# Optimization experiments

Measured on AMD Instinct MI355X. Metric: run time of the kernel, lower is better.

Reference implementation:

```python
import jax, jax.numpy as jnp
import numpy as np

E = 8        # num_workers / experts
D = 1024     # decoder_embed_dim
F = 4096     # decoder_ffn_embed_dim
S, B = 2048, 2
LN_EPS = 1e-5


def setup_inputs() -> dict:
    key = jax.random.key(0)
    ks = jax.random.split(key, 8)
    scale_in = 1.0 / np.sqrt(D)
    scale_ff = 1.0 / np.sqrt(F)
    return {
        "input_features": jax.random.normal(ks[0], (S, B, D), dtype=jnp.float32),
        "centroids": jax.random.normal(ks[1], (E, D), dtype=jnp.float32) * scale_in,  # Linear(D, E, bias=False) weight
        "ln_g": jnp.ones((E, D), dtype=jnp.float32),
        "ln_b": jnp.zeros((E, D), dtype=jnp.float32),
        "W1": jax.random.normal(ks[2], (E, D, F), dtype=jnp.float32) * scale_in,
        "b1": jax.random.normal(ks[3], (E, F), dtype=jnp.float32) * 0.01,
        "W2": jax.random.normal(ks[4], (E, F, D), dtype=jnp.float32) * scale_ff,  # original zero-inits; random for non-trivial reference
        "b2": jax.random.normal(ks[5], (E, D), dtype=jnp.float32) * 0.01,
    }


def _moe_forward(input_features, centroids, ln_g, ln_b, W1, b1, W2, b2):
    s, b, d = input_features.shape
    # [S,B,D] -> transpose(0,1) -> [B,S,D] -> flatten tokens
    x = jnp.swapaxes(input_features, 0, 1).reshape(-1, d)  # [T, D]
    # fp32 gating, top-1 (greedy) assignment; BASE layer does NOT scale by gate prob
    logits = x.astype(jnp.float32) @ centroids.astype(jnp.float32).T  # [T, E]
    assign = jnp.argmax(logits, axis=-1)                              # [T]
    onehot = jax.nn.one_hot(assign, E, dtype=x.dtype)                 # [T, E]
    # dispatch: zero out tokens not assigned to expert e  -> [E, T, D]
    disp = jnp.einsum("te,td->etd", onehot, x)
    # expert-local MoESublayer: xs + ff2(relu(ff1(LN(xs))))
    mu = disp.mean(-1, keepdims=True)
    var = disp.var(-1, keepdims=True)
    xn = (disp - mu) * jax.lax.rsqrt(var + LN_EPS)
    xn = xn * ln_g[:, None, :] + ln_b[:, None, :]
    h = jax.nn.relu(jnp.einsum("etd,edf->etf", xn, W1) + b1[:, None, :])
    y = jnp.einsum("etf,efd->etd", h, W2) + b2[:, None, :]
    y = disp + y  # residual
    # combine: pick assigned expert's output per token (sort+all2all+inverse-sort == identity permutation here)
    out = jnp.einsum("te,etd->td", onehot, y)  # [T, D]
    return jnp.swapaxes(out.reshape(b, s, d), 0, 1)  # back to [S, B, D]


def reference(input_features, centroids, ln_g, ln_b, W1, b1, W2, b2):
    return _moe_forward(input_features, centroids, ln_g, ln_b, W1, b1, W2, b2)
```

## Files before the change

kernel.cpp:

```cpp
#include <hip/hip_runtime.h>
#include <hip/hip_bf16.h>

#define E_ 8
#define D_ 1024
#define F_ 4096
#define S_ 2048
#define B_ 2
#define T_ 4096
#define LN_EPS 1e-5f
#define MAXTAB 40

typedef __attribute__((ext_vector_type(8))) short short8;
typedef __attribute__((ext_vector_type(4))) float f32x4;

__device__ __forceinline__ unsigned short f2bf(float f) {
  __hip_bfloat16 h = __float2bfloat16(f);
  return *reinterpret_cast<unsigned short*>(&h);
}

__device__ __forceinline__ void gload_lds16(const void* g, void* l) {
  __builtin_amdgcn_global_load_lds((const __attribute__((address_space(1))) void*)g,
                                   (__attribute__((address_space(3))) void*)l,
                                   16, 0, 0);
}

__global__ __launch_bounds__(256) void gate_kernel(const float* __restrict__ x,
    const float* __restrict__ cent, int* __restrict__ assign_, int* __restrict__ counts) {
  int token = blockIdx.x * 4 + (threadIdx.x >> 6);
  int lane = threadIdx.x & 63;
  int s = token & (S_ - 1);
  int b = token >> 11;
  const float* xr = x + ((size_t)s * B_ + b) * D_;
  float acc[E_];
#pragma unroll
  for (int e = 0; e < E_; ++e) acc[e] = 0.f;
#pragma unroll
  for (int c = 0; c < 4; ++c) {
    f32x4 xv = *(const f32x4*)(xr + c * 256 + lane * 4);
#pragma unroll
    for (int e = 0; e < E_; ++e) {
      f32x4 cv = *(const f32x4*)(cent + e * D_ + c * 256 + lane * 4);
      acc[e] += xv.x * cv.x + xv.y * cv.y + xv.z * cv.z + xv.w * cv.w;
    }
  }
#pragma unroll
  for (int off = 32; off > 0; off >>= 1) {
#pragma unroll
    for (int e = 0; e < E_; ++e) acc[e] += __shfl_down(acc[e], off);
  }
  if (lane == 0) {
    int best = 0; float bv = acc[0];
#pragma unroll
    for (int e = 1; e < E_; ++e) if (acc[e] > bv) { bv = acc[e]; best = e; }
    assign_[token] = best;
    atomicAdd(&counts[best], 1);
  }
}

__global__ void prefix_kernel(const int* __restrict__ counts, int* __restrict__ offs,
                              int* __restrict__ cursor, int* __restrict__ tab) {
  if (threadIdx.x == 0) {
    int s = 0, t = 0;
    for (int e = 0; e < E_; ++e) {
      offs[e] = s; cursor[e] = s;
      int nb = (counts[e] + 127) >> 7;
      for (int m = 0; m < nb; ++m) tab[t++] = (e << 16) | m;
      s += counts[e];
    }
    offs[E_] = s;
    for (; t < MAXTAB; ++t) tab[t] = -1;
  }
}

__global__ __launch_bounds__(256) void ln_scatter_kernel(const float* __restrict__ x,
    const float* __restrict__ g_, const float* __restrict__ bb_,
    const float* __restrict__ b2_,
    const int* __restrict__ assign_, int* __restrict__ cursor,
    int* __restrict__ perm, unsigned short* __restrict__ Xb,
    float* __restrict__ outp) {
  int token = blockIdx.x * 4 + (threadIdx.x >> 6);
  int lane = threadIdx.x & 63;
  int s = token & (S_ - 1), b = token >> 11;
  const float* xr = x + ((size_t)s * B_ + b) * D_;
  float* orow = outp + ((size_t)s * B_ + b) * D_;
  float v[16];
  float sum = 0.f, sq = 0.f;
#pragma unroll
  for (int c = 0; c < 4; ++c) {
    f32x4 xv = *(const f32x4*)(xr + c * 256 + lane * 4);
    v[c * 4 + 0] = xv.x; v[c * 4 + 1] = xv.y; v[c * 4 + 2] = xv.z; v[c * 4 + 3] = xv.w;
    sum += xv.x + xv.y + xv.z + xv.w;
    sq += xv.x * xv.x + xv.y * xv.y + xv.z * xv.z + xv.w * xv.w;
  }
#pragma unroll
  for (int off = 32; off > 0; off >>= 1) {
    sum += __shfl_down(sum, off);
    sq += __shfl_down(sq, off);
  }
  sum = __shfl(sum, 0); sq = __shfl(sq, 0);
  float mu = sum * (1.f / D_);
  float var = sq * (1.f / D_) - mu * mu;
  float rstd = rsqrtf(var + LN_EPS);
  int e = assign_[token];
  int slot = 0;
  if (lane == 0) { slot = atomicAdd(&cursor[e], 1); perm[slot] = token; }
  slot = __shfl(slot, 0);
  unsigned short* dst = Xb + (size_t)slot * D_;
#pragma unroll
  for (int c = 0; c < 4; ++c) {
    int d = c * 256 + lane * 4;
    f32x4 gv = *(const f32x4*)(g_ + e * D_ + d);
    f32x4 bv = *(const f32x4*)(bb_ + e * D_ + d);
    f32x4 b2v = *(const f32x4*)(b2_ + e * D_ + d);
    ushort4 o;
    o.x = f2bf((v[c * 4 + 0] - mu) * rstd * gv.x + bv.x);
    o.y = f2bf((v[c * 4 + 1] - mu) * rstd * gv.y + bv.y);
    o.z = f2bf((v[c * 4 + 2] - mu) * rstd * gv.z + bv.z);
    o.w = f2bf((v[c * 4 + 3] - mu) * rstd * gv.w + bv.w);
    *(ushort4*)(dst + d) = o;
    f32x4 oi;
    oi.x = v[c * 4 + 0] + b2v.x; oi.y = v[c * 4 + 1] + b2v.y;
    oi.z = v[c * 4 + 2] + b2v.z; oi.w = v[c * 4 + 3] + b2v.w;
    *(f32x4*)(orow + d) = oi;
  }
}

template <int K, int N, int MODE, int KSPLIT>
__global__ __launch_bounds__(256) void moe_gemm_kernel(
    const unsigned short* __restrict__ A,
    const float* __restrict__ W,
    const float* __restrict__ bias,
    const int* __restrict__ offs,
    const int* __restrict__ tab,
    const int* __restrict__ perm,
    void* __restrict__ outp) {
  const int tentry = tab[blockIdx.y];
  if (tentry < 0) return;
  const int e = tentry >> 16;
  const int m0 = (tentry & 0xffff) << 7;
  const int off = offs[e];
  const int cnt = offs[e + 1] - off;
  const int n0 = blockIdx.x * 128;
  const int kstart = blockIdx.z * (K / KSPLIT);
  constexpr int NSTEP = (K / KSPLIT) / 32;

  const int tid = threadIdx.x;
  const int lane = tid & 63;
  const int wave = tid >> 6;

  __shared__ __align__(16) unsigned short lA[4096];
  __shared__ __align__(16) unsigned short lB[4096];

  const int ar = tid & 127;
  const int aq0 = tid >> 7;
  const int arow = off + min(m0 + ar, cnt - 1);
  const unsigned short* ap = A + (size_t)arow * K + kstart;
  unsigned short* ldst0 = lA + (0 * 256 + wave * 64) * 8;
  unsigned short* ldst1 = lA + (1 * 256 + wave * 64) * 8;

  const int bq = wave;
  const int bn = (tid & 63) * 2;
  const float* wp = W + (size_t)e * K * N + (size_t)(kstart + bq * 8) * N + n0 + bn;
  unsigned short* bdst = lB + bq * 1024 + bn * 8;

  f32x4 acc[4][4] = {};
  const int wr = (wave >> 1) * 64;
  const int wc = (wave & 1) * 64;
  const int fr = lane & 15;
  const int fq = lane >> 4;
  const unsigned short* fA = lA + fq * 1024 + (wr + fr) * 8;
  const unsigned short* fB = lB + fq * 1024 + (wc + fr) * 8;

  float2 br[8];
#pragma unroll
  for (int j = 0; j < 8; ++j) br[j] = *(const float2*)(wp + (size_t)j * N);

  for (int s = 0; s < NSTEP; ++s) {
    __syncthreads();
    short8 c0, c1;
#pragma unroll
    for (int j = 0; j < 8; ++j) {
      c0[j] = (short)f2bf(br[j].x);
      c1[j] = (short)f2bf(br[j].y);
    }
    *(short8*)(bdst) = c0;
    *(short8*)(bdst + 8) = c1;
    gload_lds16(ap + s * 32 + aq0 * 8, ldst0);
    gload_lds16(ap + s * 32 + (aq0 + 2) * 8, ldst1);
    __syncthreads();
    short8 af[4], bf[4];
#pragma unroll
    for (int m = 0; m < 4; ++m) af[m] = *(const short8*)(fA + m * 128);
#pragma unroll
    for (int n = 0; n < 4; ++n) bf[n] = *(const short8*)(fB + n * 128);
    if (s + 1 < NSTEP) {
      const float* wp2 = wp + (size_t)(s + 1) * 32 * N;
#pragma unroll
      for (int j = 0; j < 8; ++j) br[j] = *(const float2*)(wp2 + (size_t)j * N);
    }
#pragma unroll
    for (int m = 0; m < 4; ++m) {
#pragma unroll
      for (int n = 0; n < 4; ++n)
        acc[m][n] = __builtin_amdgcn_mfma_f32_16x16x32_bf16(af[m], bf[n], acc[m][n], 0, 0, 0);
    }
  }

  if (MODE == 0) {
    unsigned short* Hout = (unsigned short*)outp;
    float bv[4];
#pragma unroll
    for (int n = 0; n < 4; ++n) bv[n] = bias[e * N + n0 + wc + n * 16 + fr];
#pragma unroll
    for (int m = 0; m < 4; ++m) {
#pragma unroll
      for (int j = 0; j < 4; ++j) {
        int rg = m0 + wr + m * 16 + fq * 4 + j;
        if (rg < cnt) {
          size_t base = (size_t)(off + rg) * N;
#pragma unroll
          for (int n = 0; n < 4; ++n) {
            float hv = acc[m][n][j] + bv[n];
            hv = fmaxf(hv, 0.f);
            Hout[base + n0 + wc + n * 16 + fr] = f2bf(hv);
          }
        }
      }
    }
  } else {
    float* Out = (float*)outp;
#pragma unroll
    for (int m = 0; m < 4; ++m) {
#pragma unroll
      for (int j = 0; j < 4; ++j) {
        int rg = m0 + wr + m * 16 + fq * 4 + j;
        if (rg < cnt) {
          int token = perm[off + rg];
          size_t base = ((size_t)(token & (S_ - 1)) * B_ + (token >> 11)) * (size_t)D_;
#pragma unroll
          for (int n = 0; n < 4; ++n)
            atomicAdd(&Out[base + n0 + wc + n * 16 + fr], acc[m][n][j]);
        }
      }
    }
  }
}

extern "C" void kernel_launch(void* const* d_in, const int* in_sizes, int n_in,
                              void* d_out, int out_size, void* d_ws, size_t ws_size,
                              hipStream_t stream) {
  const float* x    = (const float*)d_in[0];
  const float* cent = (const float*)d_in[1];
  const float* lng  = (const float*)d_in[2];
  const float* lnb  = (const float*)d_in[3];
  const float* W1   = (const float*)d_in[4];
  const float* b1   = (const float*)d_in[5];
  const float* W2   = (const float*)d_in[6];
  const float* b2   = (const float*)d_in[7];
  float* out = (float*)d_out;

  char* ws = (char*)d_ws;
  int* counts  = (int*)(ws + 0);
  int* offs    = (int*)(ws + 64);
  int* cursor  = (int*)(ws + 128);
  int* tab     = (int*)(ws + 256);
  int* perm    = (int*)(ws + 4096);
  int* assign_ = (int*)(ws + 4096 + 4 * T_);
  unsigned short* Xb = (unsigned short*)(ws + ((size_t)1 << 16));
  unsigned short* H  = (unsigned short*)(ws + ((size_t)1 << 24));

  if (ws_size < ((size_t)1 << 26)) return;

  hipMemsetAsync(counts, 0, 64, stream);
  gate_kernel<<<T_ / 4, 256, 0, stream>>>(x, cent, assign_, counts);
  prefix_kernel<<<1, 64, 0, stream>>>(counts, offs, cursor, tab);
  ln_scatter_kernel<<<T_ / 4, 256, 0, stream>>>(x, lng, lnb, b2, assign_, cursor, perm, Xb, out);
  moe_gemm_kernel<D_, F_, 0, 1><<<dim3(F_ / 128, MAXTAB, 1), 256, 0, stream>>>(
      Xb, W1, b1, offs, tab, perm, (void*)H);
  moe_gemm_kernel<F_, D_, 1, 2><<<dim3(D_ / 128, MAXTAB, 2), 256, 0, stream>>>(
      H, W2, nullptr, offs, tab, perm, (void*)out);
}
```

Before: 348.2 us.

## Fuse gating into LN scatter with fixed-capacity buckets and double-buffer GEMM LDS

Merges the gate and LN/scatter kernels into one pass that computes logits, picks an expert, claims a slot in a per-expert fixed-capacity bucket (CAP=1024) and writes the normalized bf16 row, which removes one read of x and the assign round trip. The GEMM kernel now double-buffers A and B tiles in LDS and prefetches the next k-step while running MFMAs, so it needs one barrier per step instead of two. The B load pattern changes to scalar strided loads per lane. The fixed capacity assumes no expert gets more than 1024 tokens; a heavier expert would overflow its bucket and be wrong.

```diff
diff --git a/kernel.cpp b/kernel.cpp
--- a/kernel.cpp
+++ b/kernel.cpp
@@ -7,6 +7,7 @@
 #define S_ 2048
 #define B_ 2
 #define T_ 4096
+#define CAP 1024
 #define LN_EPS 1e-5f
 #define MAXTAB 40
 
@@ -24,66 +25,22 @@
                                    16, 0, 0);
 }
 
-__global__ __launch_bounds__(256) void gate_kernel(const float* __restrict__ x,
-    const float* __restrict__ cent, int* __restrict__ assign_, int* __restrict__ counts) {
-  int token = blockIdx.x * 4 + (threadIdx.x >> 6);
-  int lane = threadIdx.x & 63;
-  int s = token & (S_ - 1);
-  int b = token >> 11;
-  const float* xr = x + ((size_t)s * B_ + b) * D_;
-  float acc[E_];
-#pragma unroll
-  for (int e = 0; e < E_; ++e) acc[e] = 0.f;
-#pragma unroll
-  for (int c = 0; c < 4; ++c) {
-    f32x4 xv = *(const f32x4*)(xr + c * 256 + lane * 4);
-#pragma unroll
-    for (int e = 0; e < E_; ++e) {
-      f32x4 cv = *(const f32x4*)(cent + e * D_ + c * 256 + lane * 4);
-      acc[e] += xv.x * cv.x + xv.y * cv.y + xv.z * cv.z + xv.w * cv.w;
-    }
-  }
-#pragma unroll
-  for (int off = 32; off > 0; off >>= 1) {
-#pragma unroll
-    for (int e = 0; e < E_; ++e) acc[e] += __shfl_down(acc[e], off);
-  }
-  if (lane == 0) {
-    int best = 0; float bv = acc[0];
-#pragma unroll
-    for (int e = 1; e < E_; ++e) if (acc[e] > bv) { bv = acc[e]; best = e; }
-    assign_[token] = best;
-    atomicAdd(&counts[best], 1);
-  }
-}
-
-__global__ void prefix_kernel(const int* __restrict__ counts, int* __restrict__ offs,
-                              int* __restrict__ cursor, int* __restrict__ tab) {
-  if (threadIdx.x == 0) {
-    int s = 0, t = 0;
-    for (int e = 0; e < E_; ++e) {
-      offs[e] = s; cursor[e] = s;
-      int nb = (counts[e] + 127) >> 7;
-      for (int m = 0; m < nb; ++m) tab[t++] = (e << 16) | m;
-      s += counts[e];
-    }
-    offs[E_] = s;
-    for (; t < MAXTAB; ++t) tab[t] = -1;
-  }
-}
-
-__global__ __launch_bounds__(256) void ln_scatter_kernel(const float* __restrict__ x,
+__global__ __launch_bounds__(256) void gate_ln_kernel(
+    const float* __restrict__ x, const float* __restrict__ cent,
     const float* __restrict__ g_, const float* __restrict__ bb_,
     const float* __restrict__ b2_,
-    const int* __restrict__ assign_, int* __restrict__ cursor,
-    int* __restrict__ perm, unsigned short* __restrict__ Xb,
-    float* __restrict__ outp) {
+    int* __restrict__ counts, int* __restrict__ perm,
+    unsigned short* __restrict__ Xb, float* __restrict__ outp) {
   int token = blockIdx.x * 4 + (threadIdx.x >> 6);
   int lane = threadIdx.x & 63;
   int s = token & (S_ - 1), b = token >> 11;
   const float* xr = x + ((size_t)s * B_ + b) * D_;
   float* orow = outp + ((size_t)s * B_ + b) * D_;
+
   float v[16];
+  float acc[E_];
+#pragma unroll
+  for (int e = 0; e < E_; ++e) acc[e] = 0.f;
   float sum = 0.f, sq = 0.f;
 #pragma unroll
   for (int c = 0; c < 4; ++c) {
@@ -91,21 +48,34 @@
     v[c * 4 + 0] = xv.x; v[c * 4 + 1] = xv.y; v[c * 4 + 2] = xv.z; v[c * 4 + 3] = xv.w;
     sum += xv.x + xv.y + xv.z + xv.w;
     sq += xv.x * xv.x + xv.y * xv.y + xv.z * xv.z + xv.w * xv.w;
+#pragma unroll
+    for (int e = 0; e < E_; ++e) {
+      f32x4 cv = *(const f32x4*)(cent + e * D_ + c * 256 + lane * 4);
+      acc[e] += xv.x * cv.x + xv.y * cv.y + xv.z * cv.z + xv.w * cv.w;
+    }
   }
 #pragma unroll
   for (int off = 32; off > 0; off >>= 1) {
     sum += __shfl_down(sum, off);
     sq += __shfl_down(sq, off);
-  }
+#pragma unroll
+    for (int e = 0; e < E_; ++e) acc[e] += __shfl_down(acc[e], off);
+  }
+  int best = 0, slot = 0;
+  if (lane == 0) {
+    float bv = acc[0];
+#pragma unroll
+    for (int e = 1; e < E_; ++e) if (acc[e] > bv) { bv = acc[e]; best = e; }
+    slot = atomicAdd(&counts[best], 1);
+    perm[best * CAP + slot] = token;
+  }
+  best = __shfl(best, 0); slot = __shfl(slot, 0);
   sum = __shfl(sum, 0); sq = __shfl(sq, 0);
   float mu = sum * (1.f / D_);
   float var = sq * (1.f / D_) - mu * mu;
   float rstd = rsqrtf(var + LN_EPS);
-  int e = assign_[token];
-  int slot = 0;
-  if (lane == 0) { slot = atomicAdd(&cursor[e], 1); perm[slot] = token; }
-  slot = __shfl(slot, 0);
-  unsigned short* dst = Xb + (size_t)slot * D_;
+  int e = best;
+  unsigned short* dst = Xb + (size_t)(e * CAP + slot) * D_;
 #pragma unroll
   for (int c = 0; c < 4; ++c) {
     int d = c * 256 + lane * 4;
@@ -125,11 +95,27 @@
   }
 }
 
+__global__ void prefix_kernel(const int* __restrict__ counts, int* __restrict__ offs,
+                              int* __restrict__ tab) {
+  if (threadIdx.x == 0) {
+    int s = 0, t = 0;
+    for (int e = 0; e < E_; ++e) {
+      offs[e] = s;
+      int nb = (counts[e] + 127) >> 7;
+      for (int m = 0; m < nb; ++m) tab[t++] = (e << 16) | m;
+      s += counts[e];
+    }
+    offs[E_] = s;
+    for (; t < MAXTAB; ++t) tab[t] = -1;
+  }
+}
+
 template <int K, int N, int MODE, int KSPLIT>
 __global__ __launch_bounds__(256) void moe_gemm_kernel(
     const unsigned short* __restrict__ A,
     const float* __restrict__ W,
     const float* __restrict__ bias,
+    const int* __restrict__ counts,
     const int* __restrict__ offs,
     const int* __restrict__ tab,
     const int* __restrict__ perm,
@@ -138,8 +124,10 @@
   if (tentry < 0) return;
   const int e = tentry >> 16;
   const int m0 = (tentry & 0xffff) << 7;
-  const int off = offs[e];
-  const int cnt = offs[e + 1] - off;
+  const int cnt = counts[e];
+  if (m0 >= cnt) return;
+  const int aoff = (MODE == 0) ? e * CAP : offs[e];
+  const int hoff = offs[e];
   const int n0 = blockIdx.x * 128;
   const int kstart = blockIdx.z * (K / KSPLIT);
   constexpr int NSTEP = (K / KSPLIT) / 32;
@@ -148,62 +136,67 @@
   const int lane = tid & 63;
   const int wave = tid >> 6;
 
-  __shared__ __align__(16) unsigned short lA[4096];
-  __shared__ __align__(16) unsigned short lB[4096];
+  __shared__ __align__(16) unsigned short lA[2][4096];
+  __shared__ __align__(16) unsigned short lB[2][4096];
 
   const int ar = tid & 127;
-  const int aq0 = tid >> 7;
-  const int arow = off + min(m0 + ar, cnt - 1);
-  const unsigned short* ap = A + (size_t)arow * K + kstart;
-  unsigned short* ldst0 = lA + (0 * 256 + wave * 64) * 8;
-  unsigned short* ldst1 = lA + (1 * 256 + wave * 64) * 8;
-
-  const int bq = wave;
-  const int bn = (tid & 63) * 2;
-  const float* wp = W + (size_t)e * K * N + (size_t)(kstart + bq * 8) * N + n0 + bn;
-  unsigned short* bdst = lB + bq * 1024 + bn * 8;
+  const int aq = tid >> 7;
+  const int arow = aoff + min(m0 + ar, cnt - 1);
+  const unsigned short* asrc = A + (size_t)arow * K + kstart + aq * 8;
+
+  const float* wsrc = W + (size_t)e * K * N + (size_t)(kstart + wave * 8) * N + n0 + lane;
 
   f32x4 acc[4][4] = {};
   const int wr = (wave >> 1) * 64;
   const int wc = (wave & 1) * 64;
   const int fr = lane & 15;
   const int fq = lane >> 4;
-  const unsigned short* fA = lA + fq * 1024 + (wr + fr) * 8;
-  const unsigned short* fB = lB + fq * 1024 + (wc + fr) * 8;
-
-  float2 br[8];
-#pragma unroll
-  for (int j = 0; j < 8; ++j) br[j] = *(const float2*)(wp + (size_t)j * N);
-
-  for (int s = 0; s < NSTEP; ++s) {
+
+  float bA[8], bB[8];
+#pragma unroll
+  for (int j = 0; j < 8; ++j) { bA[j] = wsrc[(size_t)j * N]; bB[j] = wsrc[(size_t)j * N + 64]; }
+  gload_lds16(asrc, (char*)&lA[0][0] + wave * 1024);
+  gload_lds16(asrc + 16, (char*)&lA[0][0] + (4 + wave) * 1024);
+  {
+    short8 c0, c1;
+#pragma unroll
+    for (int j = 0; j < 8; ++j) { c0[j] = (short)f2bf(bA[j]); c1[j] = (short)f2bf(bB[j]); }
+    *(short8*)&lB[0][(wave * 128 + lane) * 8] = c0;
+    *(short8*)&lB[0][(wave * 128 + lane + 64) * 8] = c1;
+  }
+  __syncthreads();
+
+  for (int t = 0; t < NSTEP; ++t) {
+    const int cur = t & 1, nxt = cur ^ 1;
+    if (t + 1 < NSTEP) {
+      const float* wn = wsrc + (size_t)(t + 1) * 32 * N;
+#pragma unroll
+      for (int j = 0; j < 8; ++j) { bA[j] = wn[(size_t)j * N]; bB[j] = wn[(size_t)j * N + 64]; }
+      const unsigned short* an = asrc + (t + 1) * 32;
+      gload_lds16(an, (char*)&lA[nxt][0] + wave * 1024);
+      gload_lds16(an + 16, (char*)&lA[nxt][0] + (4 + wave) * 1024);
+    }
+    short8 af[4], bf4[4];
+#pragma unroll
+    for (int m = 0; m < 4; ++m)
+      af[m] = *(const short8*)&lA[cur][fq * 1024 + (wr + m * 16 + fr) * 8];
+#pragma unroll
+    for (int n = 0; n < 4; ++n)
+      bf4[n] = *(const short8*)&lB[cur][fq * 1024 + (wc + n * 16 + fr) * 8];
+#pragma unroll
+    for (int m = 0; m < 4; ++m) {
+#pragma unroll
+      for (int n = 0; n < 4; ++n)
+        acc[m][n] = __builtin_amdgcn_mfma_f32_16x16x32_bf16(af[m], bf4[n], acc[m][n], 0, 0, 0);
+    }
+    if (t + 1 < NSTEP) {
+      short8 c0, c1;
+#pragma unroll
+      for (int j = 0; j < 8; ++j) { c0[j] = (short)f2bf(bA[j]); c1[j] = (short)f2bf(bB[j]); }
+      *(short8*)&lB[nxt][(wave * 128 + lane) * 8] = c0;
+      *(short8*)&lB[nxt][(wave * 128 + lane + 64) * 8] = c1;
+    }
     __syncthreads();
-    short8 c0, c1;
-#pragma unroll
-    for (int j = 0; j < 8; ++j) {
-      c0[j] = (short)f2bf(br[j].x);
-      c1[j] = (short)f2bf(br[j].y);
-    }
-    *(short8*)(bdst) = c0;
-    *(short8*)(bdst + 8) = c1;
-    gload_lds16(ap + s * 32 + aq0 * 8, ldst0);
-    gload_lds16(ap + s * 32 + (aq0 + 2) * 8, ldst1);
-    __syncthreads();
-    short8 af[4], bf[4];
-#pragma unroll
-    for (int m = 0; m < 4; ++m) af[m] = *(const short8*)(fA + m * 128);
-#pragma unroll
-    for (int n = 0; n < 4; ++n) bf[n] = *(const short8*)(fB + n * 128);
-    if (s + 1 < NSTEP) {
-      const float* wp2 = wp + (size_t)(s + 1) * 32 * N;
-#pragma unroll
-      for (int j = 0; j < 8; ++j) br[j] = *(const float2*)(wp2 + (size_t)j * N);
-    }
-#pragma unroll
-    for (int m = 0; m < 4; ++m) {
-#pragma unroll
-      for (int n = 0; n < 4; ++n)
-        acc[m][n] = __builtin_amdgcn_mfma_f32_16x16x32_bf16(af[m], bf[n], acc[m][n], 0, 0, 0);
-    }
   }
 
   if (MODE == 0) {
@@ -217,7 +210,7 @@
       for (int j = 0; j < 4; ++j) {
         int rg = m0 + wr + m * 16 + fq * 4 + j;
         if (rg < cnt) {
-          size_t base = (size_t)(off + rg) * N;
+          size_t base = (size_t)(hoff + rg) * N;
 #pragma unroll
           for (int n = 0; n < 4; ++n) {
             float hv = acc[m][n][j] + bv[n];
@@ -235,7 +228,7 @@
       for (int j = 0; j < 4; ++j) {
         int rg = m0 + wr + m * 16 + fq * 4 + j;
         if (rg < cnt) {
-          int token = perm[off + rg];
+          int token = perm[e * CAP + rg];
           size_t base = ((size_t)(token & (S_ - 1)) * B_ + (token >> 11)) * (size_t)D_;
 #pragma unroll
           for (int n = 0; n < 4; ++n)
@@ -260,23 +253,20 @@
   float* out = (float*)d_out;
 
   char* ws = (char*)d_ws;
-  int* counts  = (int*)(ws + 0);
-  int* offs    = (int*)(ws + 64);
-  int* cursor  = (int*)(ws + 128);
-  int* tab     = (int*)(ws + 256);
-  int* perm    = (int*)(ws + 4096);
-  int* assign_ = (int*)(ws + 4096 + 4 * T_);
-  unsigned short* Xb = (unsigned short*)(ws + ((size_t)1 << 16));
-  unsigned short* H  = (unsigned short*)(ws + ((size_t)1 << 24));
+  int* counts = (int*)(ws + 0);
+  int* offs   = (int*)(ws + 64);
+  int* tab    = (int*)(ws + 256);
+  int* perm   = (int*)(ws + 4096);
+  unsigned short* Xb = (unsigned short*)(ws + ((size_t)1 << 18));
+  unsigned short* H  = (unsigned short*)(ws + ((size_t)1 << 25));
 
   if (ws_size < ((size_t)1 << 26)) return;
 
   hipMemsetAsync(counts, 0, 64, stream);
-  gate_kernel<<<T_ / 4, 256, 0, stream>>>(x, cent, assign_, counts);
-  prefix_kernel<<<1, 64, 0, stream>>>(counts, offs, cursor, tab);
-  ln_scatter_kernel<<<T_ / 4, 256, 0, stream>>>(x, lng, lnb, b2, assign_, cursor, perm, Xb, out);
+  gate_ln_kernel<<<T_ / 4, 256, 0, stream>>>(x, cent, lng, lnb, b2, counts, perm, Xb, out);
+  prefix_kernel<<<1, 64, 0, stream>>>(counts, offs, tab);
   moe_gemm_kernel<D_, F_, 0, 1><<<dim3(F_ / 128, MAXTAB, 1), 256, 0, stream>>>(
-      Xb, W1, b1, offs, tab, perm, (void*)H);
+      Xb, W1, b1, counts, offs, tab, perm, (void*)H);
   moe_gemm_kernel<F_, D_, 1, 2><<<dim3(D_ / 128, MAXTAB, 2), 256, 0, stream>>>(
-      H, W2, nullptr, offs, tab, perm, (void*)out);
-}
+      H, W2, nullptr, counts, offs, tab, perm, (void*)out);
+}
```

New measurement: 285.5 us. 18.0% less time.
